# Optimization experiments

Measured on AMD Instinct MI355X. Metric: run time of the kernel, lower is better.

## Reference

```python
import jax, jax.numpy as jnp
import numpy as np

B, T, C = 8, 2048, 1024
E = 8            # num_experts (= world_size in the original)
K = 2            # top-k
CAP_FACTOR = 1.25
CAPACITY = int(T / E * CAP_FACTOR)  # 320, per (expert, batch-row)
DFF = 4 * C


def setup_inputs() -> dict:
    key = jax.random.key(0)
    ks = jax.random.split(key, 4)
    x = jax.random.normal(ks[0], (B, T, C), dtype=jnp.float32)
    Wg = jax.random.normal(ks[1], (C, E), dtype=jnp.float32) * (C ** -0.5)
    bg = jnp.zeros((E,), dtype=jnp.float32)
    W1 = jax.random.normal(ks[2], (E, C, DFF), dtype=jnp.float32) * (C ** -0.5)
    b1 = jnp.zeros((E, DFF), dtype=jnp.float32)
    W2 = jax.random.normal(ks[3], (E, DFF, C), dtype=jnp.float32) * (DFF ** -0.5)
    b2 = jnp.zeros((E, C), dtype=jnp.float32)
    return {"x": x, "Wg": Wg, "bg": bg, "W1": W1, "b1": b1, "W2": W2, "b2": b2}


def reference(x, Wg, bg, W1, b1, W2, b2):
    # Router: linear + softmax, then top-k gating
    probs = jax.nn.softmax(jnp.einsum('btc,ce->bte', x, Wg) + bg, axis=-1)  # [B,T,E]
    topk_p, topk_e = jax.lax.top_k(probs, K)                               # [B,T,K]

    S = T * K  # one "assignment" per (token, k-slot), row-major (t, k) order
    e_flat = topk_e.reshape(B, S)                      # expert id per assignment
    p_flat = topk_p.reshape(B, S)

    # Position of each assignment within its (batch-row, expert) group,
    # ordered by token position then k-slot (matches nonzero() row-major order).
    onehot = (e_flat[..., None] == jnp.arange(E)).astype(jnp.int32)        # [B,S,E]
    pos_all = jnp.cumsum(onehot, axis=1) - 1                                # [B,S,E]
    pos = jnp.take_along_axis(pos_all, e_flat[..., None], axis=2)[..., 0]   # [B,S]
    keep = pos < CAPACITY                               # overflow tokens are dropped

    # Dispatch tokens into padded per-(expert,row) buffers: [E,B,CAPACITY,C]
    x_rep = jnp.repeat(x, K, axis=1)                    # [B,S,C], assignment order
    b_idx = jnp.broadcast_to(jnp.arange(B)[:, None], (B, S))
    pos_scat = jnp.where(keep, pos, CAPACITY)           # out-of-range -> dropped
    dispatch = jnp.zeros((E, B, CAPACITY, C), dtype=x.dtype)
    dispatch = dispatch.at[e_flat, b_idx, pos_scat].set(x_rep, mode='drop')

    # Grouped expert FFN (padding rows are zeros; their outputs are never read back)
    h = jax.nn.relu(jnp.einsum('ebsc,ech->ebsh', dispatch, W1) + b1[:, None, None, :])
    y = jnp.einsum('ebsh,ehc->ebsc', h, W2) + b2[:, None, None, :]

    # Combine: gather back, scale by gate prob (dropped tokens -> padding_val 0)
    gathered = y[e_flat, b_idx, jnp.clip(pos, 0, CAPACITY - 1)]             # [B,S,C]
    out = gathered * jnp.where(keep, p_flat, 0.0)[..., None]
    return out.reshape(B, T, K, C).sum(axis=2)          # sum over k assignments
```

## Files before the change

kernel.cpp:

```cpp
#include <hip/hip_runtime.h>
#include <stdint.h>

#define B_ 8
#define T_ 2048
#define C_ 1024
#define E_ 8
#define K_ 2
#define CAP_ 320
#define DFF_ 4096
#define S_ (T_*K_)
#define NTOK (B_*T_)
#define ROWS_PER_E (B_*CAP_)

typedef __attribute__((ext_vector_type(8))) short short8;
typedef __attribute__((ext_vector_type(4))) float floatx4;

__device__ __forceinline__ unsigned short f2bf(float f) {
  union { float f; unsigned u; } v; v.f = f;
  unsigned r = v.u + 0x7fffu + ((v.u >> 16) & 1u);
  return (unsigned short)(r >> 16);
}
__device__ __forceinline__ float bf2f(unsigned short h) {
  union { unsigned u; float f; } v; v.u = ((unsigned)h) << 16;
  return v.f;
}

#define GLOAD16(g, l) __builtin_amdgcn_global_load_lds( \
    (const __attribute__((address_space(1))) void*)(g), \
    (__attribute__((address_space(3))) void*)(l), 16, 0, 0)

#define BARRIER() asm volatile("s_barrier" ::: "memory")

__global__ void router_kernel(const float* __restrict__ x, const float* __restrict__ Wg,
                              const float* __restrict__ bg,
                              int* __restrict__ topk_e, float* __restrict__ topk_p)
{
  int token = (int)((blockIdx.x * blockDim.x + threadIdx.x) >> 6);
  int lane = threadIdx.x & 63;
  if (token >= NTOK) return;
  const float* xr = x + (size_t)token * C_;
  double acc[E_];
  #pragma unroll
  for (int e = 0; e < E_; ++e) acc[e] = 0.0;
  for (int c = lane; c < C_; c += 64) {
    double xv = (double)xr[c];
    const float4* w4 = (const float4*)(Wg + (size_t)c * E_);
    float4 wa = w4[0], wb = w4[1];
    acc[0] += xv * (double)wa.x; acc[1] += xv * (double)wa.y;
    acc[2] += xv * (double)wa.z; acc[3] += xv * (double)wa.w;
    acc[4] += xv * (double)wb.x; acc[5] += xv * (double)wb.y;
    acc[6] += xv * (double)wb.z; acc[7] += xv * (double)wb.w;
  }
  #pragma unroll
  for (int off = 32; off; off >>= 1) {
    #pragma unroll
    for (int e = 0; e < E_; ++e) acc[e] += __shfl_down(acc[e], off, 64);
  }
  if (lane == 0) {
    double lg[E_];
    double mx = -1e300;
    #pragma unroll
    for (int e = 0; e < E_; ++e) { lg[e] = acc[e] + (double)bg[e]; mx = fmax(mx, lg[e]); }
    double se = 0.0, pr[E_];
    #pragma unroll
    for (int e = 0; e < E_; ++e) { pr[e] = exp(lg[e] - mx); se += pr[e]; }
    #pragma unroll
    for (int e = 0; e < E_; ++e) pr[e] /= se;
    int e0 = 0;
    #pragma unroll
    for (int e = 1; e < E_; ++e) if (pr[e] > pr[e0]) e0 = e;
    int e1 = -1;
    #pragma unroll
    for (int e = 0; e < E_; ++e) {
      if (e == e0) continue;
      if (e1 < 0 || pr[e] > pr[e1]) e1 = e;
    }
    topk_e[token*2+0] = e0; topk_p[token*2+0] = (float)pr[e0];
    topk_e[token*2+1] = e1; topk_p[token*2+1] = (float)pr[e1];
  }
}

__global__ void scan_kernel(const int* __restrict__ topk_e,
                            int* __restrict__ pos_arr, int* __restrict__ slot_src,
                            int* __restrict__ counts)
{
  const int b = blockIdx.x;
  const int tid = threadIdx.x;
  const int PT = S_ / 256;
  __shared__ int cnt[256][E_];
  int e_loc[16];
  int local[E_];
  #pragma unroll
  for (int e = 0; e < E_; ++e) local[e] = 0;
  const int* te = topk_e + (size_t)b * S_;
  for (int j = 0; j < PT; ++j) {
    int e = te[tid*PT + j];
    e_loc[j] = e;
    local[e]++;
  }
  #pragma unroll
  for (int e = 0; e < E_; ++e) cnt[tid][e] = local[e];
  __syncthreads();
  if (tid < E_) {
    int run = 0;
    for (int i = 0; i < 256; ++i) { int v = cnt[i][tid]; cnt[i][tid] = run; run += v; }
    counts[tid*B_ + b] = run;
  }
  __syncthreads();
  int base[E_];
  #pragma unroll
  for (int e = 0; e < E_; ++e) base[e] = cnt[tid][e];
  for (int j = 0; j < PT; ++j) {
    int e = e_loc[j];
    int p = base[e]++;
    int s = tid*PT + j;
    if (p < CAP_) {
      pos_arr[(size_t)b*S_ + s] = p;
      slot_src[((size_t)e*B_ + b)*CAP_ + p] = s >> 1;
    } else {
      pos_arr[(size_t)b*S_ + s] = -1;
    }
  }
}

__global__ void transpose_conv_kernel(const float* __restrict__ in, unsigned short* __restrict__ out,
                                      int R, int Cc)
{
  __shared__ float tile[64][33];
  const int e = blockIdx.z;
  const float* ine = in + (size_t)e * R * Cc;
  unsigned short* oute = out + (size_t)e * R * Cc;
  const int c0 = blockIdx.x * 32, r0 = blockIdx.y * 64;
  const int tx = threadIdx.x & 7, ty = threadIdx.x >> 3;
  #pragma unroll
  for (int p = 0; p < 2; ++p) {
    const int rr = p*32 + ty;
    float4 v = *(const float4*)(ine + (size_t)(r0 + rr) * Cc + c0 + tx*4);
    tile[rr][tx*4+0] = v.x; tile[rr][tx*4+1] = v.y;
    tile[rr][tx*4+2] = v.z; tile[rr][tx*4+3] = v.w;
  }
  __syncthreads();
  short8 s;
  #pragma unroll
  for (int j = 0; j < 8; ++j) s[j] = (short)f2bf(tile[tx*8+j][ty]);
  *(short8*)(oute + (size_t)(c0 + ty) * R + r0 + tx*8) = s;
}

__global__ void dispatch_kernel(const float* __restrict__ x, const int* __restrict__ slot_src,
                                const int* __restrict__ counts, unsigned short* __restrict__ Xd,
                                int e_base, int nexp)
{
  int row = (int)((blockIdx.x * blockDim.x + threadIdx.x) >> 6);
  int lane = threadIdx.x & 63;
  int total = nexp * B_ * CAP_;
  if (row >= total) return;
  int el = row / (B_*CAP_);
  int rem = row - el*(B_*CAP_);
  int b = rem / CAP_, slot = rem - b*CAP_;
  int eg = e_base + el;
  int cnt = counts[eg*B_ + b]; if (cnt > CAP_) cnt = CAP_;
  unsigned short* orow = Xd + (size_t)row * C_;
  if (slot < cnt) {
    int t = slot_src[((size_t)eg*B_ + b)*CAP_ + slot];
    const float4* xr = (const float4*)(x + ((size_t)b*T_ + t)*C_);
    #pragma unroll
    for (int i = 0; i < C_/256; ++i) {
      float4 v = xr[i*64 + lane];
      ushort4 o;
      o.x = f2bf(v.x); o.y = f2bf(v.y); o.z = f2bf(v.z); o.w = f2bf(v.w);
      ((ushort4*)orow)[i*64 + lane] = o;
    }
  } else {
    ushort4 z; z.x = z.y = z.z = z.w = 0;
    #pragma unroll
    for (int i = 0; i < C_/256; ++i) ((ushort4*)orow)[i*64 + lane] = z;
  }
}

template<int RELU>
__global__ __launch_bounds__(512) void gemm256_kernel(
    const unsigned short* __restrict__ A,
    const unsigned short* __restrict__ BT,
    const float* __restrict__ bias,
    unsigned short* __restrict__ Out0,
    unsigned short* __restrict__ Out1,
    int M, int N, int Kfull, int klen, int tilesPerSplit, int nwg)
{
  __shared__ __align__(16) unsigned short lds[65536];
  const int NT = N >> 8, MT = M >> 8;
  const int bid = blockIdx.x;
  const int wg = (bid & 7) * (nwg >> 3) + (bid >> 3);
  const int sp  = wg / tilesPerSplit;
  const int wgr = wg - sp * tilesPerSplit;
  const int e  = wgr / (MT*NT);
  const int r2 = wgr - e*(MT*NT);
  const int mt = r2 / NT, nt = r2 - mt*NT;
  const int k0 = sp * klen;
  const unsigned short* Ae = A + (size_t)e * M * Kfull;
  const unsigned short* Be = BT + (size_t)e * N * Kfull;
  const float* be = bias ? (bias + (size_t)e * N) : nullptr;
  unsigned short* Oe = (sp == 0 ? Out0 : Out1) + (size_t)e * M * N;
  const int m0 = mt*256, n0 = nt*256;

  const int tid = threadIdx.x, lane = tid & 63, w = tid >> 6;
  const int wr = w >> 2, wc = w & 3;

  floatx4 acc[8][4];
  #pragma unroll
  for (int i = 0; i < 8; ++i)
    #pragma unroll
    for (int j = 0; j < 4; ++j) acc[i][j] = (floatx4){0.f, 0.f, 0.f, 0.f};

  const int r0s = tid >> 2;
  const int p0s = ((tid & 3) ^ ((r0s >> 1) & 3)) * 8;
  const unsigned short* gA0 = Ae + (size_t)(m0 + r0s)*Kfull + k0 + p0s;
  const unsigned short* gA1 = gA0 + (size_t)128*Kfull;
  const unsigned short* gB0 = Be + (size_t)(n0 + r0s)*Kfull + k0 + p0s;
  const unsigned short* gB1 = gB0 + (size_t)128*Kfull;
  const int la0 = w*512, la1 = 4096 + w*512;

  const int fr = lane & 15, kq = lane >> 4;
  const int kqs = ((kq ^ ((fr >> 1) & 3)) * 8);
  const int aBase = (wr*128 + fr)*32 + kqs;
  const int bBase = 32768 + (wc*64 + fr)*32 + kqs;

  const int nk = klen >> 6;

#define STAGE_AH(h) do { int _s = (h)&3; size_t _k = (size_t)((h)>>1)*64 + ((h)&1)*32; \
    GLOAD16(gA0 + _k, lds + _s*8192 + la0); \
    GLOAD16(gA1 + _k, lds + _s*8192 + la1); } while(0)
#define STAGE_BH(h) do { int _s = (h)&3; size_t _k = (size_t)((h)>>1)*64 + ((h)&1)*32; \
    GLOAD16(gB0 + _k, lds + 32768 + _s*8192 + la0); \
    GLOAD16(gB1 + _k, lds + 32768 + _s*8192 + la1); } while(0)

  STAGE_AH(0); STAGE_BH(0);
  STAGE_AH(1); STAGE_BH(1);
  STAGE_AH(2); STAGE_BH(2);
  asm volatile("s_waitcnt vmcnt(4)" ::: "memory");
  BARRIER();

  for (int t = 0; t < nk; ++t) {
    const int s0 = (2*t) & 3, s1 = (2*t+1) & 3;
    const unsigned short* sA0 = lds + s0*8192;
    const unsigned short* sA1 = lds + s1*8192;
    short8 af[4], bfr[4];

    #pragma unroll
    for (int nf = 0; nf < 4; ++nf) bfr[nf] = *(const short8*)(sA0 + bBase + nf*512);
    #pragma unroll
    for (int mf = 0; mf < 4; ++mf) af[mf] = *(const short8*)(sA0 + aBase + mf*512);
    if (t + 1 < nk) STAGE_AH(2*(t+1)+1);
    BARRIER();
    asm volatile("s_waitcnt lgkmcnt(0)" ::: "memory");
    __builtin_amdgcn_s_setprio(1);
    #pragma unroll
    for (int mf = 0; mf < 4; ++mf)
      #pragma unroll
      for (int nf = 0; nf < 4; ++nf)
        acc[mf][nf] = __builtin_amdgcn_mfma_f32_16x16x32_bf16(af[mf], bfr[nf], acc[mf][nf], 0, 0, 0);
    __builtin_amdgcn_s_setprio(0);
    BARRIER();

    #pragma unroll
    for (int mf = 0; mf < 4; ++mf) af[mf] = *(const short8*)(sA0 + aBase + (mf+4)*512);
    if (t + 1 < nk) STAGE_BH(2*(t+1)+1);
    BARRIER();
    asm volatile("s_waitcnt lgkmcnt(0)" ::: "memory");
    __builtin_amdgcn_s_setprio(1);
    #pragma unroll
    for (int mf = 0; mf < 4; ++mf)
      #pragma unroll
      for (int nf = 0; nf < 4; ++nf)
        acc[mf+4][nf] = __builtin_amdgcn_mfma_f32_16x16x32_bf16(af[mf], bfr[nf], acc[mf+4][nf], 0, 0, 0);
    __builtin_amdgcn_s_setprio(0);
    BARRIER();

    #pragma unroll
    for (int nf = 0; nf < 4; ++nf) bfr[nf] = *(const short8*)(sA1 + bBase + nf*512);
    #pragma unroll
    for (int mf = 0; mf < 4; ++mf) af[mf] = *(const short8*)(sA1 + aBase + mf*512);
    if (t + 2 < nk) STAGE_AH(2*(t+2));
    BARRIER();
    asm volatile("s_waitcnt lgkmcnt(0)" ::: "memory");
    __builtin_amdgcn_s_setprio(1);
    #pragma unroll
    for (int mf = 0; mf < 4; ++mf)
      #pragma unroll
      for (int nf = 0; nf < 4; ++nf)
        acc[mf][nf] = __builtin_amdgcn_mfma_f32_16x16x32_bf16(af[mf], bfr[nf], acc[mf][nf], 0, 0, 0);
    __builtin_amdgcn_s_setprio(0);
    BARRIER();

    #pragma unroll
    for (int mf = 0; mf < 4; ++mf) af[mf] = *(const short8*)(sA1 + aBase + (mf+4)*512);
    if (t + 2 < nk) STAGE_BH(2*(t+2));
    BARRIER();
    asm volatile("s_waitcnt lgkmcnt(0)" ::: "memory");
    __builtin_amdgcn_s_setprio(1);
    #pragma unroll
    for (int mf = 0; mf < 4; ++mf)
      #pragma unroll
      for (int nf = 0; nf < 4; ++nf)
        acc[mf+4][nf] = __builtin_amdgcn_mfma_f32_16x16x32_bf16(af[mf], bfr[nf], acc[mf+4][nf], 0, 0, 0);
    __builtin_amdgcn_s_setprio(0);

    if (t + 1 < nk) {
      if (t + 2 < nk) asm volatile("s_waitcnt vmcnt(4)" ::: "memory");
      else            asm volatile("s_waitcnt vmcnt(0)" ::: "memory");
      BARRIER();
    }
  }
#undef STAGE_AH
#undef STAGE_BH

  const int col = lane & 15, rbase = (lane >> 4) * 4;
  #pragma unroll
  for (int mf = 0; mf < 8; ++mf) {
    const int gr0 = m0 + wr*128 + mf*16 + rbase;
    #pragma unroll
    for (int nf = 0; nf < 4; ++nf) {
      const int gc = n0 + wc*64 + nf*16 + col;
      const float bv = be ? be[gc] : 0.f;
      #pragma unroll
      for (int r = 0; r < 4; ++r) {
        float v = acc[mf][nf][r] + bv;
        if (RELU) v = fmaxf(v, 0.f);
        Oe[(size_t)(gr0 + r)*N + gc] = f2bf(v);
      }
    }
  }
}

__global__ void combine_kernel(const unsigned short* __restrict__ Y0,
                               const unsigned short* __restrict__ Y1,
                               const float* __restrict__ b2c,
                               const int* __restrict__ topk_e, const float* __restrict__ topk_p,
                               const int* __restrict__ pos_arr, float* __restrict__ out)
{
  int token = (int)((blockIdx.x * blockDim.x + threadIdx.x) >> 6);
  int lane = threadIdx.x & 63;
  if (token >= NTOK) return;
  int b = token / T_, t = token - b*T_;
  int s0 = b*S_ + t*2;
  float acc[16];
  #pragma unroll
  for (int i = 0; i < 16; ++i) acc[i] = 0.f;
  #pragma unroll
  for (int k = 0; k < 2; ++k) {
    int pos = pos_arr[s0 + k];
    if (pos < 0) continue;
    int e = topk_e[s0 + k];
    float p = topk_p[s0 + k];
    size_t rowoff = (((size_t)e*B_ + b)*CAP_ + pos) * C_;
    const unsigned short* yr0 = Y0 + rowoff;
    const unsigned short* yr1 = Y1 ? (Y1 + rowoff) : nullptr;
    const float* bb = b2c ? (b2c + (size_t)e * C_) : nullptr;
    #pragma unroll
    for (int i = 0; i < 4; ++i) {
      ushort4 v = ((const ushort4*)yr0)[i*64 + lane];
      float s0v = bf2f(v.x), s1v = bf2f(v.y), s2v = bf2f(v.z), s3v = bf2f(v.w);
      if (yr1) {
        ushort4 u = ((const ushort4*)yr1)[i*64 + lane];
        s0v += bf2f(u.x); s1v += bf2f(u.y); s2v += bf2f(u.z); s3v += bf2f(u.w);
      }
      if (bb) {
        float4 bv = ((const float4*)bb)[i*64 + lane];
        s0v += bv.x; s1v += bv.y; s2v += bv.z; s3v += bv.w;
      }
      acc[i*4+0] += p * s0v;
      acc[i*4+1] += p * s1v;
      acc[i*4+2] += p * s2v;
      acc[i*4+3] += p * s3v;
    }
  }
  float4* orow = (float4*)(out + (size_t)token * C_);
  #pragma unroll
  for (int i = 0; i < 4; ++i) {
    float4 o;
    o.x = acc[i*4+0]; o.y = acc[i*4+1]; o.z = acc[i*4+2]; o.w = acc[i*4+3];
    orow[i*64 + lane] = o;
  }
}

extern "C" void kernel_launch(void* const* d_in, const int* in_sizes, int n_in,
                              void* d_out, int out_size, void* d_ws, size_t ws_size,
                              hipStream_t stream)
{
  const float* x  = (const float*)d_in[0];
  const float* Wg = (const float*)d_in[1];
  const float* bg = (const float*)d_in[2];
  const float* W1 = (const float*)d_in[3];
  const float* b1 = (const float*)d_in[4];
  const float* W2 = (const float*)d_in[5];
  const float* b2 = (const float*)d_in[6];
  float* out = (float*)d_out;

  char* ws = (char*)d_ws;
  size_t off = 0;
  auto alloc = [&](size_t bytes) -> char* {
    char* p = ws + off;
    off = (off + bytes + 255) & ~(size_t)255;
    return p;
  };
  int*   topk_e  = (int*)  alloc((size_t)NTOK * K_ * 4);
  float* topk_p  = (float*)alloc((size_t)NTOK * K_ * 4);
  int*   pos_arr = (int*)  alloc((size_t)B_ * S_ * 4);
  int*   slot_src= (int*)  alloc((size_t)E_ * B_ * CAP_ * 4);
  int*   counts  = (int*)  alloc((size_t)E_ * B_ * 4);
  unsigned short* Ybuf = (unsigned short*)alloc((size_t)E_ * ROWS_PER_E * C_ * 2);
  size_t fixed = off;
  const size_t perE = (size_t)C_ * DFF_ * 2
                    + (size_t)ROWS_PER_E * C_ * 2
                    + (size_t)ROWS_PER_E * DFF_ * 2
                    + 3 * 256;
  int k = 8;
  while (k > 1 && fixed + (size_t)k * perE > ws_size) k >>= 1;
  unsigned short* Wt = (unsigned short*)alloc((size_t)k * C_ * DFF_ * 2);
  unsigned short* Xd = (unsigned short*)alloc((size_t)k * ROWS_PER_E * C_ * 2);
  unsigned short* Hb = (unsigned short*)alloc((size_t)k * ROWS_PER_E * DFF_ * 2);

  router_kernel<<<NTOK/4, 256, 0, stream>>>(x, Wg, bg, topk_e, topk_p);
  scan_kernel<<<B_, 256, 0, stream>>>(topk_e, pos_arr, slot_src, counts);

  const bool splitK2 = (k == 8);

  for (int eb = 0; eb < E_; eb += k) {
    transpose_conv_kernel<<<dim3(DFF_/32, C_/64, k), 256, 0, stream>>>(
        W1 + (size_t)eb * C_ * DFF_, Wt, C_, DFF_);
    dispatch_kernel<<<(k * ROWS_PER_E) / 4, 256, 0, stream>>>(x, slot_src, counts, Xd, eb, k);
    {
      int tiles = k * (ROWS_PER_E/256) * (DFF_/256);
      gemm256_kernel<1><<<tiles, 512, 0, stream>>>(
          Xd, Wt, b1 + (size_t)eb * DFF_, Hb, Hb, ROWS_PER_E, DFF_, C_, C_, tiles, tiles);
    }
    transpose_conv_kernel<<<dim3(C_/32, DFF_/64, k), 256, 0, stream>>>(
        W2 + (size_t)eb * DFF_ * C_, Wt, DFF_, C_);
    {
      int tiles = k * (ROWS_PER_E/256) * (C_/256);
      if (splitK2) {
        gemm256_kernel<0><<<2*tiles, 512, 0, stream>>>(
            Hb, Wt, nullptr, Ybuf, Xd, ROWS_PER_E, C_, DFF_, DFF_/2, tiles, 2*tiles);
      } else {
        gemm256_kernel<0><<<tiles, 512, 0, stream>>>(
            Hb, Wt, b2 + (size_t)eb * C_, Ybuf + (size_t)eb * ROWS_PER_E * C_,
            Ybuf + (size_t)eb * ROWS_PER_E * C_, ROWS_PER_E, C_, DFF_, DFF_, tiles, tiles);
      }
    }
  }

  combine_kernel<<<NTOK/4, 256, 0, stream>>>(
      Ybuf, splitK2 ? Xd : nullptr, splitK2 ? b2 : nullptr,
      topk_e, topk_p, pos_arr, out);
}
```

Before: 578.5 us.

## Software-pipeline LDS fragment loads and drop most barriers in GEMM main loop

Rewrites the GEMM inner loop so each k-tile's A-high and second-stage fragments are read from LDS into separate registers ahead of time. Partial lgkmcnt waits replace the full drains, and most of the per-phase s_barriers are removed, which lets LDS reads overlap with MFMA work. sched_barrier markers pin the intended instruction order. This needs more VGPRs for the extra fragment registers, and it relies on the remaining barrier being enough to keep the staged LDS buffers from being overwritten while still being read.

```diff
diff --git a/kernel.cpp b/kernel.cpp
--- a/kernel.cpp
+++ b/kernel.cpp
@@ -30,6 +30,7 @@
     (__attribute__((address_space(3))) void*)(l), 16, 0, 0)
 
 #define BARRIER() asm volatile("s_barrier" ::: "memory")
+#define SCHEDB() __builtin_amdgcn_sched_barrier(0)
 
 __global__ void router_kernel(const float* __restrict__ x, const float* __restrict__ Wg,
                               const float* __restrict__ bg,
@@ -243,66 +244,73 @@
     const int s0 = (2*t) & 3, s1 = (2*t+1) & 3;
     const unsigned short* sA0 = lds + s0*8192;
     const unsigned short* sA1 = lds + s1*8192;
-    short8 af[4], bfr[4];
-
-    #pragma unroll
-    for (int nf = 0; nf < 4; ++nf) bfr[nf] = *(const short8*)(sA0 + bBase + nf*512);
-    #pragma unroll
-    for (int mf = 0; mf < 4; ++mf) af[mf] = *(const short8*)(sA0 + aBase + mf*512);
-    if (t + 1 < nk) STAGE_AH(2*(t+1)+1);
-    BARRIER();
-    asm volatile("s_waitcnt lgkmcnt(0)" ::: "memory");
+    short8 rB0[4], rA0lo[4], rA0hi[4], rB1[4], rA1lo[4], rA1hi[4];
+
+    #pragma unroll
+    for (int nf = 0; nf < 4; ++nf) rB0[nf] = *(const short8*)(sA0 + bBase + nf*512);
+    #pragma unroll
+    for (int mf = 0; mf < 4; ++mf) rA0lo[mf] = *(const short8*)(sA0 + aBase + mf*512);
+    SCHEDB();
+    #pragma unroll
+    for (int mf = 0; mf < 4; ++mf) rA0hi[mf] = *(const short8*)(sA0 + aBase + (mf+4)*512);
+    if (t + 1 < nk) STAGE_AH(2*t+3);
+    SCHEDB();
+    asm volatile("s_waitcnt lgkmcnt(4)" ::: "memory");
+    SCHEDB();
     __builtin_amdgcn_s_setprio(1);
     #pragma unroll
     for (int mf = 0; mf < 4; ++mf)
       #pragma unroll
       for (int nf = 0; nf < 4; ++nf)
-        acc[mf][nf] = __builtin_amdgcn_mfma_f32_16x16x32_bf16(af[mf], bfr[nf], acc[mf][nf], 0, 0, 0);
+        acc[mf][nf] = __builtin_amdgcn_mfma_f32_16x16x32_bf16(rA0lo[mf], rB0[nf], acc[mf][nf], 0, 0, 0);
     __builtin_amdgcn_s_setprio(0);
+    SCHEDB();
+
+    #pragma unroll
+    for (int nf = 0; nf < 4; ++nf) rB1[nf] = *(const short8*)(sA1 + bBase + nf*512);
+    #pragma unroll
+    for (int mf = 0; mf < 4; ++mf) rA1lo[mf] = *(const short8*)(sA1 + aBase + mf*512);
+    if (t + 1 < nk) STAGE_BH(2*t+3);
+    SCHEDB();
+    asm volatile("s_waitcnt lgkmcnt(8)" ::: "memory");
+    SCHEDB();
     BARRIER();
-
-    #pragma unroll
-    for (int mf = 0; mf < 4; ++mf) af[mf] = *(const short8*)(sA0 + aBase + (mf+4)*512);
-    if (t + 1 < nk) STAGE_BH(2*(t+1)+1);
-    BARRIER();
-    asm volatile("s_waitcnt lgkmcnt(0)" ::: "memory");
     __builtin_amdgcn_s_setprio(1);
     #pragma unroll
     for (int mf = 0; mf < 4; ++mf)
       #pragma unroll
       for (int nf = 0; nf < 4; ++nf)
-        acc[mf+4][nf] = __builtin_amdgcn_mfma_f32_16x16x32_bf16(af[mf], bfr[nf], acc[mf+4][nf], 0, 0, 0);
+        acc[mf+4][nf] = __builtin_amdgcn_mfma_f32_16x16x32_bf16(rA0hi[mf], rB0[nf], acc[mf+4][nf], 0, 0, 0);
     __builtin_amdgcn_s_setprio(0);
-    BARRIER();
-
-    #pragma unroll
-    for (int nf = 0; nf < 4; ++nf) bfr[nf] = *(const short8*)(sA1 + bBase + nf*512);
-    #pragma unroll
-    for (int mf = 0; mf < 4; ++mf) af[mf] = *(const short8*)(sA1 + aBase + mf*512);
-    if (t + 2 < nk) STAGE_AH(2*(t+2));
-    BARRIER();
-    asm volatile("s_waitcnt lgkmcnt(0)" ::: "memory");
+    SCHEDB();
+
+    #pragma unroll
+    for (int mf = 0; mf < 4; ++mf) rA1hi[mf] = *(const short8*)(sA1 + aBase + (mf+4)*512);
+    if (t + 2 < nk) STAGE_AH(2*t+4);
+    SCHEDB();
+    asm volatile("s_waitcnt lgkmcnt(4)" ::: "memory");
+    SCHEDB();
     __builtin_amdgcn_s_setprio(1);
     #pragma unroll
     for (int mf = 0; mf < 4; ++mf)
       #pragma unroll
       for (int nf = 0; nf < 4; ++nf)
-        acc[mf][nf] = __builtin_amdgcn_mfma_f32_16x16x32_bf16(af[mf], bfr[nf], acc[mf][nf], 0, 0, 0);
+        acc[mf][nf] = __builtin_amdgcn_mfma_f32_16x16x32_bf16(rA1lo[mf], rB1[nf], acc[mf][nf], 0, 0, 0);
     __builtin_amdgcn_s_setprio(0);
-    BARRIER();
-
-    #pragma unroll
-    for (int mf = 0; mf < 4; ++mf) af[mf] = *(const short8*)(sA1 + aBase + (mf+4)*512);
-    if (t + 2 < nk) STAGE_BH(2*(t+2));
-    BARRIER();
+    SCHEDB();
+
+    if (t + 2 < nk) STAGE_BH(2*t+4);
+    SCHEDB();
     asm volatile("s_waitcnt lgkmcnt(0)" ::: "memory");
+    SCHEDB();
     __builtin_amdgcn_s_setprio(1);
     #pragma unroll
     for (int mf = 0; mf < 4; ++mf)
       #pragma unroll
       for (int nf = 0; nf < 4; ++nf)
-        acc[mf+4][nf] = __builtin_amdgcn_mfma_f32_16x16x32_bf16(af[mf], bfr[nf], acc[mf+4][nf], 0, 0, 0);
+        acc[mf+4][nf] = __builtin_amdgcn_mfma_f32_16x16x32_bf16(rA1hi[mf], rB1[nf], acc[mf+4][nf], 0, 0, 0);
     __builtin_amdgcn_s_setprio(0);
+    SCHEDB();
 
     if (t + 1 < nk) {
       if (t + 2 < nk) asm volatile("s_waitcnt vmcnt(4)" ::: "memory");
```

Measured after the change: 570.0 us. No clear change (-1.5%).
